# Kernel optimization log

Measured on AMD Instinct MI355X. Metric: run time of the kernel, lower is better.

The kernel has to match this reference:

```python
import jax, jax.numpy as jnp
import numpy as np

TEMPERATURE = 0.07
EPS = 1e-12  # F.normalize default eps

def _l2norm(x):
    n = jnp.linalg.norm(x, axis=1, keepdims=True)
    return x / jnp.maximum(n, EPS)

def setup_inputs() -> dict:
    key = jax.random.key(0)
    k1, k2 = jax.random.split(key)
    N, D = 16384, 256
    return {
        "feat_local": jax.random.normal(k1, (N, D), dtype=jnp.float32),
        "feat_global": jax.random.normal(k2, (N, D), dtype=jnp.float32),
    }

def reference(feat_local, feat_global):
    fl = _l2norm(feat_local)
    fg = _l2norm(feat_global)
    # [N, N] similarity matrix scaled by temperature
    sim = jnp.einsum('nd,md->nm', fl, fg) / TEMPERATURE
    pos_sim = jnp.diagonal(sim)
    loss = -pos_sim + jax.scipy.special.logsumexp(sim, axis=1)
    return loss.mean()
```

## Files before the change

### kernel.cpp

```cpp
#include <hip/hip_runtime.h>
#include <hip/hip_bf16.h>

#define NROWS 16384
#define DIM   256
#define SEGS  8
#define BN    128
#define NT    ((NROWS / SEGS) / BN)
#define INVT  14.285714285714286f
#define C1f   20.60992915555662f
#define LN2f  0.6931471805599453f

typedef __attribute__((ext_vector_type(8)))  int   int8v;
typedef __attribute__((ext_vector_type(16))) float f32x16;

#define SCALE1 0x7F7F7F7F

__global__ __launch_bounds__(256) void norm_diag_kernel(
    const float* __restrict__ fl, const float* __restrict__ fg,
    unsigned char* __restrict__ A, unsigned char* __restrict__ B,
    float* __restrict__ diag, float* __restrict__ out)
{
    int tid  = threadIdx.x;
    int wave = tid >> 6, lane = tid & 63;
    int row  = blockIdx.x * 4 + wave;
    if (blockIdx.x == 0 && tid == 0) out[0] = 0.0f;

    float4 xl = ((const float4*)(fl + (size_t)row * DIM))[lane];
    float4 xg = ((const float4*)(fg + (size_t)row * DIM))[lane];
    float ssl = xl.x*xl.x + xl.y*xl.y + xl.z*xl.z + xl.w*xl.w;
    float ssg = xg.x*xg.x + xg.y*xg.y + xg.z*xg.z + xg.w*xg.w;
    for (int m = 1; m < 64; m <<= 1) {
        ssl += __shfl_xor(ssl, m, 64);
        ssg += __shfl_xor(ssg, m, 64);
    }
    float il = 1.0f / fmaxf(sqrtf(ssl), 1e-12f);
    float ig = 1.0f / fmaxf(sqrtf(ssg), 1e-12f);
    float nl0 = xl.x*il, nl1 = xl.y*il, nl2 = xl.z*il, nl3 = xl.w*il;
    float ng0 = xg.x*ig, ng1 = xg.y*ig, ng2 = xg.z*ig, ng3 = xg.w*ig;

    int pa = __builtin_amdgcn_cvt_pk_fp8_f32(nl0 * C1f, nl1 * C1f, 0, false);
    pa     = __builtin_amdgcn_cvt_pk_fp8_f32(nl2 * C1f, nl3 * C1f, pa, true);
    int pb = __builtin_amdgcn_cvt_pk_fp8_f32(ng0, ng1, 0, false);
    pb     = __builtin_amdgcn_cvt_pk_fp8_f32(ng2, ng3, pb, true);
    ((int*)(A + (size_t)row * DIM))[lane] = pa;

    {
        int kcb = lane >> 2;
        int b4  = lane & 3;
        unsigned chunk = (unsigned)((row >> 7) * 2048 + ((row >> 6) & 1) * 1024
                                    + kcb * 64 + (row & 63));
        ((int*)B)[chunk * 4 + b4] = pb;
    }

    float d = nl0*ng0 + nl1*ng1 + nl2*ng2 + nl3*ng3;
    for (int m = 1; m < 64; m <<= 1) d += __shfl_xor(d, m, 64);
    if (lane == 0) diag[row] = d;
}

__global__ __launch_bounds__(256, 2) void sim_lse_kernel(
    const unsigned char* __restrict__ A, const unsigned char* __restrict__ B,
    float* __restrict__ lpart)
{
    __shared__ __align__(16) unsigned char bt[2 * BN * DIM];

    int tid  = threadIdx.x;
    int lane = tid & 63;
    int l31  = lane & 31, half = lane >> 5;
    int wave = tid >> 6;
    int seg  = blockIdx.x;
    int rowBase = blockIdx.y * 256 + wave * 64;

    unsigned vb = (unsigned)(l31 * 16 + half * 2048);

    int8v af[2][4];
#pragma unroll
    for (int s = 0; s < 2; ++s) {
        const unsigned char* ap = A + (size_t)(rowBase + s*32 + l31) * DIM + half * 32;
#pragma unroll
        for (int kk = 0; kk < 4; ++kk) {
            ((int4*)&af[s][kk])[0] = *(const int4*)(ap + kk * 64);
            ((int4*)&af[s][kk])[1] = *(const int4*)(ap + kk * 64 + 16);
        }
    }

    f32x16 lv[2];
    f32x16 Z;
    f32x16 accA[2], accB[2];
#pragma unroll
    for (int r = 0; r < 16; ++r) {
        lv[0][r] = -1.0f; lv[1][r] = -1.0f;
        Z[r] = 0.0f;
        accB[0][r] = 0.0f; accB[1][r] = 0.0f;
    }

    int T0 = seg * NT;

    auto stage = [&](int T, unsigned bufo) {
        const unsigned char* g = B + (size_t)T * (BN * DIM) + (wave * 512 + lane) * 16;
        unsigned lo = bufo + (unsigned)(wave * 512) * 16;
#pragma unroll
        for (int j = 0; j < 8; ++j) {
            __builtin_amdgcn_global_load_lds(
                (const __attribute__((address_space(1))) unsigned int*)(g + j * 1024),
                (__attribute__((address_space(3))) unsigned int*)&bt[lo + j * 1024],
                16, 0, 0);
        }
    };

    auto chain = [&](f32x16 (&ac)[2], unsigned ab, unsigned offc) {
        int8v bf[4];
#pragma unroll
        for (int kk = 0; kk < 4; ++kk) {
            ((int4*)&bf[kk])[0] = *(const int4*)&bt[ab + offc + (unsigned)kk * 4096u];
            ((int4*)&bf[kk])[1] = *(const int4*)&bt[ab + offc + (unsigned)kk * 4096u + 1024u];
        }
        ac[0] = __builtin_amdgcn_mfma_scale_f32_32x32x64_f8f6f4(
            af[0][0], bf[0], Z, 0, 0, 0, SCALE1, 0, SCALE1);
        ac[1] = __builtin_amdgcn_mfma_scale_f32_32x32x64_f8f6f4(
            af[1][0], bf[0], Z, 0, 0, 0, SCALE1, 0, SCALE1);
#pragma unroll
        for (int kk = 1; kk < 4; ++kk) {
            ac[0] = __builtin_amdgcn_mfma_scale_f32_32x32x64_f8f6f4(
                af[0][kk], bf[kk], ac[0], 0, 0, 0, SCALE1, 0, SCALE1);
            ac[1] = __builtin_amdgcn_mfma_scale_f32_32x32x64_f8f6f4(
                af[1][kk], bf[kk], ac[1], 0, 0, 0, SCALE1, 0, SCALE1);
        }
    };

    auto epi = [&](f32x16 (&ac)[2]) {
#pragma unroll
        for (int s = 0; s < 2; ++s) {
            f32x16 e;
#pragma unroll
            for (int r = 0; r < 16; ++r)
                e[r] = __builtin_amdgcn_exp2f(ac[s][r]);
            lv[s] += e;
        }
    };

    stage(T0, 0);

    for (int t = 0; t < NT; ++t) {
        unsigned bufo = (t & 1) ? (unsigned)(BN * DIM) : 0u;
        __syncthreads();

        if (t + 1 < NT)
            stage(T0 + t + 1, (t & 1) ? 0u : (unsigned)(BN * DIM));

        unsigned ab = vb + bufo;
        chain(accA, ab, 0u);      epi(accB);
        chain(accB, ab, 512u);    epi(accA);
        chain(accA, ab, 16384u);  epi(accB);
        chain(accB, ab, 16896u);  epi(accA);
    }
    epi(accB);

#pragma unroll
    for (int s = 0; s < 2; ++s)
#pragma unroll
        for (int r = 0; r < 16; ++r) {
            float v = lv[s][r];
            v += __shfl_xor(v, 1, 64);
            v += __shfl_xor(v, 2, 64);
            v += __shfl_xor(v, 4, 64);
            v += __shfl_xor(v, 8, 64);
            v += __shfl_xor(v, 16, 64);
            lv[s][r] = v;
        }
    if (l31 == 0) {
#pragma unroll
        for (int s = 0; s < 2; ++s)
#pragma unroll
            for (int r = 0; r < 16; ++r) {
                int row = rowBase + s*32 + (r & 3) + 8*(r >> 2) + 4*half;
                lpart[(size_t)seg * NROWS + row] = lv[s][r];
            }
    }
}

__global__ __launch_bounds__(256) void reduce_kernel(
    const float* __restrict__ lpart, const float* __restrict__ diag,
    float* __restrict__ out)
{
    __shared__ float sm[4];
    int gtid = blockIdx.x * 256 + threadIdx.x;
    float s = 0.0f;
    for (int row = gtid; row < NROWS; row += 32 * 256) {
        float t = 0.0f;
#pragma unroll
        for (int g = 0; g < SEGS; ++g) t += lpart[(size_t)g * NROWS + row];
        s += LN2f * log2f(t) - INVT * diag[row];
    }
    for (int m = 1; m < 64; m <<= 1) s += __shfl_xor(s, m, 64);
    int wave = threadIdx.x >> 6, lane = threadIdx.x & 63;
    if (lane == 0) sm[wave] = s;
    __syncthreads();
    if (threadIdx.x == 0) {
        float tot = sm[0] + sm[1] + sm[2] + sm[3];
        atomicAdd(out, tot * (1.0f / NROWS));
    }
}

extern "C" void kernel_launch(void* const* d_in, const int* in_sizes, int n_in,
                              void* d_out, int out_size, void* d_ws, size_t ws_size,
                              hipStream_t stream) {
    const float* fl = (const float*)d_in[0];
    const float* fg = (const float*)d_in[1];
    float* out = (float*)d_out;

    char* ws = (char*)d_ws;
    unsigned char* A = (unsigned char*)ws;
    unsigned char* B = A + (size_t)NROWS * DIM;
    float* diag  = (float*)(ws + 2 * (size_t)NROWS * DIM);
    float* lpart = diag + NROWS;

    norm_diag_kernel<<<NROWS / 4, 256, 0, stream>>>(fl, fg, A, B, diag, out);
    sim_lse_kernel<<<dim3(SEGS, NROWS / 256), 256, 0, stream>>>(A, B, lpart);
    reduce_kernel<<<32, 256, 0, stream>>>(lpart, diag, out);
}
```

Measured before the change: 137.9 us.

## Switch similarity GEMM from 32x32x64 to 16x16x128 scaled FP8 MFMA tiles

Recasts the FP8 similarity MFMA from 32x32x64 to 16x16x128 scaled instructions. Each wave now computes a 4x2 grid of 16x16 output tiles per chain with two K steps instead of four, and the A-fragment, B-fragment and LDS addressing, the exp2 epilogue and the cross-lane row reduction are remapped to match. The intent is a shorter K chain per accumulator and a different MFMA throughput/latency profile, at the cost of more accumulator registers and a new fragment-layout mapping against the existing B swizzle. The initial lv offset is changed from -1 to -2 to cancel the two zero-padded columns per lane.

```diff
diff --git a/kernel.cpp b/kernel.cpp
--- a/kernel.cpp
+++ b/kernel.cpp
@@ -11,7 +11,7 @@
 #define LN2f  0.6931471805599453f
 
 typedef __attribute__((ext_vector_type(8)))  int   int8v;
-typedef __attribute__((ext_vector_type(16))) float f32x16;
+typedef __attribute__((ext_vector_type(4)))  float f32x4;
 
 #define SCALE1 0x7F7F7F7F
 
@@ -65,33 +65,38 @@
 
     int tid  = threadIdx.x;
     int lane = tid & 63;
-    int l31  = lane & 31, half = lane >> 5;
+    int l15  = lane & 15, quad = lane >> 4;
     int wave = tid >> 6;
     int seg  = blockIdx.x;
     int rowBase = blockIdx.y * 256 + wave * 64;
 
-    unsigned vb = (unsigned)(l31 * 16 + half * 2048);
-
-    int8v af[2][4];
-#pragma unroll
-    for (int s = 0; s < 2; ++s) {
-        const unsigned char* ap = A + (size_t)(rowBase + s*32 + l31) * DIM + half * 32;
-#pragma unroll
-        for (int kk = 0; kk < 4; ++kk) {
-            ((int4*)&af[s][kk])[0] = *(const int4*)(ap + kk * 64);
-            ((int4*)&af[s][kk])[1] = *(const int4*)(ap + kk * 64 + 16);
+    unsigned vb = (unsigned)(l15 * 16 + quad * 2048);
+
+    int8v af[4][2];
+#pragma unroll
+    for (int rs = 0; rs < 4; ++rs) {
+        const unsigned char* ap = A + (size_t)(rowBase + rs*16 + l15) * DIM + quad * 32;
+#pragma unroll
+        for (int ks = 0; ks < 2; ++ks) {
+            ((int4*)&af[rs][ks])[0] = *(const int4*)(ap + ks * 128);
+            ((int4*)&af[rs][ks])[1] = *(const int4*)(ap + ks * 128 + 16);
         }
     }
 
-    f32x16 lv[2];
-    f32x16 Z;
-    f32x16 accA[2], accB[2];
-#pragma unroll
-    for (int r = 0; r < 16; ++r) {
-        lv[0][r] = -1.0f; lv[1][r] = -1.0f;
-        Z[r] = 0.0f;
-        accB[0][r] = 0.0f; accB[1][r] = 0.0f;
-    }
+    f32x4 lv[4];
+    f32x4 Z4;
+    f32x4 accA[4][2], accB[4][2];
+#pragma unroll
+    for (int rs = 0; rs < 4; ++rs) {
+#pragma unroll
+        for (int r = 0; r < 4; ++r) lv[rs][r] = -2.0f;
+#pragma unroll
+        for (int cs = 0; cs < 2; ++cs)
+#pragma unroll
+            for (int r = 0; r < 4; ++r) { accB[rs][cs][r] = 0.0f; }
+    }
+#pragma unroll
+    for (int r = 0; r < 4; ++r) Z4[r] = 0.0f;
 
     int T0 = seg * NT;
 
@@ -107,35 +112,38 @@
         }
     };
 
-    auto chain = [&](f32x16 (&ac)[2], unsigned ab, unsigned offc) {
-        int8v bf[4];
-#pragma unroll
-        for (int kk = 0; kk < 4; ++kk) {
-            ((int4*)&bf[kk])[0] = *(const int4*)&bt[ab + offc + (unsigned)kk * 4096u];
-            ((int4*)&bf[kk])[1] = *(const int4*)&bt[ab + offc + (unsigned)kk * 4096u + 1024u];
-        }
-        ac[0] = __builtin_amdgcn_mfma_scale_f32_32x32x64_f8f6f4(
-            af[0][0], bf[0], Z, 0, 0, 0, SCALE1, 0, SCALE1);
-        ac[1] = __builtin_amdgcn_mfma_scale_f32_32x32x64_f8f6f4(
-            af[1][0], bf[0], Z, 0, 0, 0, SCALE1, 0, SCALE1);
-#pragma unroll
-        for (int kk = 1; kk < 4; ++kk) {
-            ac[0] = __builtin_amdgcn_mfma_scale_f32_32x32x64_f8f6f4(
-                af[0][kk], bf[kk], ac[0], 0, 0, 0, SCALE1, 0, SCALE1);
-            ac[1] = __builtin_amdgcn_mfma_scale_f32_32x32x64_f8f6f4(
-                af[1][kk], bf[kk], ac[1], 0, 0, 0, SCALE1, 0, SCALE1);
-        }
+    auto chain = [&](f32x4 (&ac)[4][2], unsigned ab, unsigned offc) {
+        int8v bf[2][2];
+#pragma unroll
+        for (int cs = 0; cs < 2; ++cs)
+#pragma unroll
+            for (int ks = 0; ks < 2; ++ks) {
+                unsigned base = ab + offc + (unsigned)cs * 256u + (unsigned)ks * 8192u;
+                ((int4*)&bf[cs][ks])[0] = *(const int4*)&bt[base];
+                ((int4*)&bf[cs][ks])[1] = *(const int4*)&bt[base + 1024u];
+            }
+#pragma unroll
+        for (int rs = 0; rs < 4; ++rs)
+#pragma unroll
+            for (int cs = 0; cs < 2; ++cs)
+                ac[rs][cs] = __builtin_amdgcn_mfma_scale_f32_16x16x128_f8f6f4(
+                    af[rs][0], bf[cs][0], Z4, 0, 0, 0, SCALE1, 0, SCALE1);
+#pragma unroll
+        for (int rs = 0; rs < 4; ++rs)
+#pragma unroll
+            for (int cs = 0; cs < 2; ++cs)
+                ac[rs][cs] = __builtin_amdgcn_mfma_scale_f32_16x16x128_f8f6f4(
+                    af[rs][1], bf[cs][1], ac[rs][cs], 0, 0, 0, SCALE1, 0, SCALE1);
     };
 
-    auto epi = [&](f32x16 (&ac)[2]) {
-#pragma unroll
-        for (int s = 0; s < 2; ++s) {
-            f32x16 e;
-#pragma unroll
-            for (int r = 0; r < 16; ++r)
-                e[r] = __builtin_amdgcn_exp2f(ac[s][r]);
-            lv[s] += e;
-        }
+    auto epi = [&](f32x4 (&ac)[4][2]) {
+#pragma unroll
+        for (int rs = 0; rs < 4; ++rs)
+#pragma unroll
+            for (int cs = 0; cs < 2; ++cs)
+#pragma unroll
+                for (int r = 0; r < 4; ++r)
+                    lv[rs][r] += __builtin_amdgcn_exp2f(ac[rs][cs][r]);
     };
 
     stage(T0, 0);
@@ -156,24 +164,23 @@
     epi(accB);
 
 #pragma unroll
-    for (int s = 0; s < 2; ++s)
-#pragma unroll
-        for (int r = 0; r < 16; ++r) {
-            float v = lv[s][r];
+    for (int rs = 0; rs < 4; ++rs)
+#pragma unroll
+        for (int r = 0; r < 4; ++r) {
+            float v = lv[rs][r];
             v += __shfl_xor(v, 1, 64);
             v += __shfl_xor(v, 2, 64);
             v += __shfl_xor(v, 4, 64);
             v += __shfl_xor(v, 8, 64);
-            v += __shfl_xor(v, 16, 64);
-            lv[s][r] = v;
+            lv[rs][r] = v;
         }
-    if (l31 == 0) {
-#pragma unroll
-        for (int s = 0; s < 2; ++s)
-#pragma unroll
-            for (int r = 0; r < 16; ++r) {
-                int row = rowBase + s*32 + (r & 3) + 8*(r >> 2) + 4*half;
-                lpart[(size_t)seg * NROWS + row] = lv[s][r];
+    if (l15 == 0) {
+#pragma unroll
+        for (int rs = 0; rs < 4; ++rs)
+#pragma unroll
+            for (int r = 0; r < 4; ++r) {
+                int row = rowBase + rs*16 + quad*4 + r;
+                lpart[(size_t)seg * NROWS + row] = lv[rs][r];
             }
     }
 }
```

Result: slower. 197.0 us (+42.8%).
